# Performance work log

Hardware: AMD Instinct MI355X
Metric: run time of the kernel (lower is better)

The kernel has to match this reference:

```python
import jax, jax.numpy as jnp
import numpy as np

N_NODES = 50000
N_EDGES = 800000
IN_FEAT = 128
HID = 64
HEADS = 4
OUT = 40
NEG_SLOPE = 0.2


def _p(key, shape, scale=0.05):
    return jax.random.normal(key, shape, dtype=jnp.float32) * scale


def setup_inputs() -> dict:
    key = jax.random.key(0)
    ks = jax.random.split(key, 20)
    HW = HID * HEADS  # 256
    inp = {
        "x": jax.random.normal(ks[0], (N_NODES, IN_FEAT), dtype=jnp.float32),
        "edge_index": jax.random.randint(ks[1], (2, N_EDGES), 0, N_NODES, dtype=jnp.int64),
        # GATConv 1: in=128 -> heads=4, C=64
        "W1": _p(ks[2], (IN_FEAT, HW)), "as1": _p(ks[3], (HEADS, HID)), "ad1": _p(ks[4], (HEADS, HID)), "b1": jnp.zeros((HW,), jnp.float32),
        # GATConv 2: in=256
        "W2": _p(ks[5], (HW, HW)), "as2": _p(ks[6], (HEADS, HID)), "ad2": _p(ks[7], (HEADS, HID)), "b2": jnp.zeros((HW,), jnp.float32),
        # GATConv 3: in=256
        "W3": _p(ks[8], (HW, HW)), "as3": _p(ks[9], (HEADS, HID)), "ad3": _p(ks[10], (HEADS, HID)), "b3": jnp.zeros((HW,), jnp.float32),
        # MLP head: Linear(256,256) + Linear(256,40)
        "Wm1": _p(ks[11], (HW, HW)), "bm1": jnp.zeros((HW,), jnp.float32),
        "Wm2": _p(ks[12], (HW, OUT)), "bm2": jnp.zeros((OUT,), jnp.float32),
    }
    return inp


def gat_conv(x, src, dst, W, a_src, a_dst, bias, num_nodes):
    """PyG GATConv: concat=True, add_self_loops=True, leaky_relu(0.2)."""
    H, C = a_src.shape
    h = (x @ W).reshape(num_nodes, H, C)            # [N,H,C]
    # per-node attention logits (computed once, gathered per edge)
    src_logit = jnp.einsum('nhc,hc->nh', h, a_src)  # [N,H]
    dst_logit = jnp.einsum('nhc,hc->nh', h, a_dst)  # [N,H]
    # add self loops
    loop = jnp.arange(num_nodes, dtype=src.dtype)
    s = jnp.concatenate([src, loop])
    d = jnp.concatenate([dst, loop])
    alpha = jax.nn.leaky_relu(src_logit[s] + dst_logit[d], NEG_SLOPE)  # [E,H]
    # segment softmax over incoming edges of each destination node
    amax = jax.ops.segment_max(alpha, d, num_segments=num_nodes)
    e = jnp.exp(alpha - amax[d])
    denom = jax.ops.segment_sum(e, d, num_segments=num_nodes)
    coef = e / denom[d]                              # [E,H]
    msg = h[s] * coef[:, :, None]                    # [E,H,C] gather+weight
    out = jax.ops.segment_sum(msg, d, num_segments=num_nodes)  # [N,H,C]
    return out.reshape(num_nodes, H * C) + bias


def reference(x, edge_index, W1, as1, ad1, b1, W2, as2, ad2, b2, W3, as3, ad3, b3, Wm1, bm1, Wm2, bm2):
    src, dst = edge_index[0], edge_index[1]
    n = x.shape[0]
    h = jax.nn.relu(gat_conv(x, src, dst, W1, as1, ad1, b1, n))
    h = jax.nn.relu(gat_conv(h, src, dst, W2, as2, ad2, b2, n))
    h = jax.nn.relu(gat_conv(h, src, dst, W3, as3, ad3, b3, n))
    h = jax.nn.relu(h @ Wm1 + bm1)
    return h @ Wm2 + bm2
```

## Files before the change

### kernel.cpp

```cpp
#include <hip/hip_runtime.h>


constexpr int NN = 50000;
constexpr int NE = 800000;
constexpr int NN_PAD = 50176;
constexpr int CAP = 48;

typedef _Float16 f16x8 __attribute__((ext_vector_type(8)));
typedef _Float16 f16x4 __attribute__((ext_vector_type(4)));
typedef float    f32x4 __attribute__((ext_vector_type(4)));

__device__ __forceinline__ void cp16(void* lds, const void* g)
{
    __builtin_amdgcn_global_load_lds(
        (const __attribute__((address_space(1))) uint32_t*)g,
        (__attribute__((address_space(3))) uint32_t*)lds, 16, 0, 0);
}

constexpr int CVT_BLKS = 944;
__global__ __launch_bounds__(256)
void prep_kernel(const float* __restrict__ W1, const float* __restrict__ W2,
                 const float* __restrict__ W3, const float* __restrict__ Wm1,
                 const float* __restrict__ Wm2,
                 _Float16* B1h, _Float16* B1l, _Float16* B2h, _Float16* B2l,
                 _Float16* B3h, _Float16* B3l, _Float16* Bmh, _Float16* Bml,
                 _Float16* Whh, _Float16* Whl,
                 const int* __restrict__ src, const int* __restrict__ dst,
                 int* __restrict__ cursor, int* __restrict__ bucket)
{
    if (blockIdx.x >= CVT_BLKS) {
        int e = ((int)blockIdx.x - CVT_BLKS) * 256 + (int)threadIdx.x;
        if (e >= NE) return;
        int d = dst[e];
        int pos = atomicAdd(&cursor[d], 1);
        if (pos < CAP) bucket[d * CAP + pos] = src[e];
        return;
    }
    int idx = blockIdx.x * 256 + (int)threadIdx.x;
    const float* W; _Float16 *H, *Lo; int K, local;
    if (idx < 32768)       { W = W1;  H = B1h; Lo = B1l; K = 128; local = idx; }
    else if (idx < 98304)  { W = W2;  H = B2h; Lo = B2l; K = 256; local = idx - 32768; }
    else if (idx < 163840) { W = W3;  H = B3h; Lo = B3l; K = 256; local = idx - 98304; }
    else if (idx < 229376) { W = Wm1; H = Bmh; Lo = Bml; K = 256; local = idx - 163840; }
    else if (idx < 241664) {
        int l = idx - 229376; int n = l >> 8, k = l & 255;
        float v = (n < 40) ? Wm2[k * 40 + n] : 0.f;
        _Float16 h = (_Float16)v;
        Whh[l] = h; Whl[l] = (_Float16)(v - (float)h);
        return;
    } else return;
    int k = local >> 8, n = local & 255;
    float v = W[local];
    _Float16 h = (_Float16)v;
    H[n * K + k] = h;
    Lo[n * K + k] = (_Float16)(v - (float)h);
}

template<bool FUSE, bool PRESPLIT, bool EMIT_SPLIT>
__global__ __launch_bounds__(512, 4)
void gemm_mfma(const float* __restrict__ A,
               const _Float16* Ah, const _Float16* Al,
               const _Float16* __restrict__ Bhi, const _Float16* __restrict__ Blo,
               const float* __restrict__ bias,
               _Float16* __restrict__ h16, _Float16* __restrict__ h16lo,
               _Float16* Oh, _Float16* Ol,
               const float* __restrict__ a_src, const float* __restrict__ a_dst,
               float* __restrict__ sl, float* __restrict__ dl,
               int M, int K)
{
    __shared__ __align__(16) _Float16 sAhi[128][32], sAlo[128][32];
    __shared__ __align__(16) _Float16 sBhi[256][32], sBlo[256][32];

    const int tid  = (int)threadIdx.x;
    const int wave = tid >> 6;
    const int mw   = wave >> 2;
    const int nw   = wave & 3;
    const int lane = tid & 63;
    const int l15  = lane & 15;
    const int quad = lane >> 4;
    const int swz  = (l15 >> 1) & 3;
    const int bm   = blockIdx.x * 128;

    f32x4 acc[4][4];
    #pragma unroll
    for (int i = 0; i < 4; ++i)
        #pragma unroll
        for (int j = 0; j < 4; ++j)
            acc[i][j] = (f32x4){0.f, 0.f, 0.f, 0.f};

    for (int k0 = 0; k0 < K; k0 += 32) {
        {
            int pos = lane & 3;
            #pragma unroll
            for (int j = 0; j < 2; ++j) {
                int rowB = wave * 32 + j * 16 + (lane >> 2);
                int c = pos ^ ((rowB >> 1) & 3);
                cp16(&sBhi[wave * 32 + j * 16][0], Bhi + (size_t)rowB * K + k0 + c * 8);
                cp16(&sBlo[wave * 32 + j * 16][0], Blo + (size_t)rowB * K + k0 + c * 8);
            }
        }
        if (PRESPLIT) {
            int pos = lane & 3;
            int rowA = wave * 16 + (lane >> 2);
            int c = pos ^ ((rowA >> 1) & 3);
            cp16(&sAhi[wave * 16][0], Ah + (size_t)(bm + rowA) * K + k0 + c * 8);
            cp16(&sAlo[wave * 16][0], Al + (size_t)(bm + rowA) * K + k0 + c * 8);
        } else {
            int r = tid >> 2, c = tid & 3;
            int grow = bm + r;
            float4 v0 = make_float4(0.f, 0.f, 0.f, 0.f), v1 = v0;
            if (grow < M) {
                v0 = *(const float4*)(A + (size_t)grow * K + k0 + c * 8);
                v1 = *(const float4*)(A + (size_t)grow * K + k0 + c * 8 + 4);
            }
            float fv[8] = {v0.x, v0.y, v0.z, v0.w, v1.x, v1.y, v1.z, v1.w};
            f16x8 h8, l8;
            #pragma unroll
            for (int u = 0; u < 8; ++u) {
                _Float16 hh = (_Float16)fv[u];
                h8[u] = hh; l8[u] = (_Float16)(fv[u] - (float)hh);
            }
            int slot = (c ^ ((r >> 1) & 3)) * 8;
            *(f16x8*)&sAhi[r][slot] = h8;
            *(f16x8*)&sAlo[r][slot] = l8;
        }
        __syncthreads();

        f16x8 bh[4], bl[4];
        #pragma unroll
        for (int nt = 0; nt < 4; ++nt) {
            int n = nw * 64 + nt * 16 + l15;
            bh[nt] = *(const f16x8*)&sBhi[n][(quad ^ swz) * 8];
            bl[nt] = *(const f16x8*)&sBlo[n][(quad ^ swz) * 8];
        }
        #pragma unroll
        for (int mt = 0; mt < 4; ++mt) {
            int m = mw * 64 + mt * 16 + l15;
            f16x8 ah = *(const f16x8*)&sAhi[m][(quad ^ swz) * 8];
            f16x8 al = *(const f16x8*)&sAlo[m][(quad ^ swz) * 8];
            #pragma unroll
            for (int nt = 0; nt < 4; ++nt) {
                acc[mt][nt] = __builtin_amdgcn_mfma_f32_16x16x32_f16(ah, bh[nt], acc[mt][nt], 0, 0, 0);
                acc[mt][nt] = __builtin_amdgcn_mfma_f32_16x16x32_f16(al, bh[nt], acc[mt][nt], 0, 0, 0);
                acc[mt][nt] = __builtin_amdgcn_mfma_f32_16x16x32_f16(ah, bl[nt], acc[mt][nt], 0, 0, 0);
            }
        }
        __syncthreads();
    }

    float aS[4], aD[4];
    if (FUSE) {
        #pragma unroll
        for (int nt = 0; nt < 4; ++nt) {
            aS[nt] = a_src[nw * 64 + nt * 16 + l15];
            aD[nt] = a_dst[nw * 64 + nt * 16 + l15];
        }
    }

    #pragma unroll
    for (int mt = 0; mt < 4; ++mt) {
        #pragma unroll
        for (int r = 0; r < 4; ++r) {
            int row = bm + mw * 64 + mt * 16 + quad * 4 + r;
            bool ok = (row < M);
            if (ok) {
                #pragma unroll
                for (int nt = 0; nt < 4; ++nt) {
                    int col = nw * 64 + nt * 16 + l15;
                    float c = acc[mt][nt][r];
                    if (EMIT_SPLIT) {
                        float v = fmaxf(c + bias[col], 0.f);
                        _Float16 hh = (_Float16)v;
                        Oh[(size_t)row * 256 + col] = hh;
                        Ol[(size_t)row * 256 + col] = (_Float16)(v - (float)hh);
                    } else {
                        _Float16 hh = (_Float16)c;
                        h16[(size_t)row * 256 + col] = hh;
                        h16lo[(size_t)row * 256 + col] = (_Float16)(c - (float)hh);
                    }
                }
            }
            if (FUSE) {
                float vs = 0.f, vd = 0.f;
                #pragma unroll
                for (int nt = 0; nt < 4; ++nt) {
                    float c = acc[mt][nt][r];
                    vs = fmaf(c, aS[nt], vs);
                    vd = fmaf(c, aD[nt], vd);
                }
                #pragma unroll
                for (int off = 8; off >= 1; off >>= 1) {
                    vs += __shfl_xor(vs, off, 64);
                    vd += __shfl_xor(vd, off, 64);
                }
                if (l15 == 0 && ok) {
                    sl[row * 4 + nw] = vs;
                    dl[row * 4 + nw] = vd;
                }
            }
        }
    }
}

__global__ __launch_bounds__(256)
void gemm_head(const _Float16* __restrict__ Ah, const _Float16* __restrict__ Al,
               const _Float16* __restrict__ Bh, const _Float16* __restrict__ Bl,
               const float* __restrict__ bias, float* __restrict__ out, int M)
{
    __shared__ _Float16 sAhi[256][40], sAlo[256][40];
    __shared__ _Float16 sBhi[48][40],  sBlo[48][40];

    const int tid  = (int)threadIdx.x;
    const int wave = tid >> 6;
    const int lane = tid & 63;
    const int l15  = lane & 15;
    const int quad = lane >> 4;
    const int bm   = blockIdx.x * 256;

    f32x4 acc[4][3];
    #pragma unroll
    for (int i = 0; i < 4; ++i)
        #pragma unroll
        for (int j = 0; j < 3; ++j)
            acc[i][j] = (f32x4){0.f, 0.f, 0.f, 0.f};

    for (int k0 = 0; k0 < 256; k0 += 32) {
        #pragma unroll
        for (int i = 0; i < 4; ++i) {
            int idx = tid + i * 256;
            int row = idx >> 2, kq = (idx & 3) * 8;
            int grow = bm + row;
            uint4 vh = {0,0,0,0}, vl = {0,0,0,0};
            if (grow < M) {
                vh = *(const uint4*)(Ah + (size_t)grow * 256 + k0 + kq);
                vl = *(const uint4*)(Al + (size_t)grow * 256 + k0 + kq);
            }
            *(uint4*)&sAhi[row][kq] = vh;
            *(uint4*)&sAlo[row][kq] = vl;
        }
        if (tid < 192) {
            int n = tid >> 2, kq = (tid & 3) * 8;
            *(uint4*)&sBhi[n][kq] = *(const uint4*)(Bh + (size_t)n * 256 + k0 + kq);
            *(uint4*)&sBlo[n][kq] = *(const uint4*)(Bl + (size_t)n * 256 + k0 + kq);
        }
        __syncthreads();

        f16x8 bh[3], bl[3];
        #pragma unroll
        for (int nt = 0; nt < 3; ++nt) {
            int n = nt * 16 + l15;
            bh[nt] = *(const f16x8*)&sBhi[n][quad * 8];
            bl[nt] = *(const f16x8*)&sBlo[n][quad * 8];
        }
        #pragma unroll
        for (int mt = 0; mt < 4; ++mt) {
            int m = wave * 64 + mt * 16 + l15;
            f16x8 ah = *(const f16x8*)&sAhi[m][quad * 8];
            f16x8 al = *(const f16x8*)&sAlo[m][quad * 8];
            #pragma unroll
            for (int nt = 0; nt < 3; ++nt) {
                acc[mt][nt] = __builtin_amdgcn_mfma_f32_16x16x32_f16(ah, bh[nt], acc[mt][nt], 0, 0, 0);
                acc[mt][nt] = __builtin_amdgcn_mfma_f32_16x16x32_f16(al, bh[nt], acc[mt][nt], 0, 0, 0);
                acc[mt][nt] = __builtin_amdgcn_mfma_f32_16x16x32_f16(ah, bl[nt], acc[mt][nt], 0, 0, 0);
            }
        }
        __syncthreads();
    }

    #pragma unroll
    for (int mt = 0; mt < 4; ++mt) {
        #pragma unroll
        for (int r = 0; r < 4; ++r) {
            int row = bm + wave * 64 + mt * 16 + quad * 4 + r;
            if (row >= M) continue;
            #pragma unroll
            for (int nt = 0; nt < 3; ++nt) {
                int col = nt * 16 + l15;
                if (col < 40)
                    out[(size_t)row * 40 + col] = acc[mt][nt][r] + bias[col];
            }
        }
    }
}

__device__ __forceinline__ float leaky02(float a) {
    return (a >= 0.f) ? a : 0.2f * a;
}

__global__ __launch_bounds__(256)
void gat_aggregate(const int* __restrict__ cursor, const int* __restrict__ bucket,
                   const float* __restrict__ sl, const float* __restrict__ dl,
                   const _Float16* __restrict__ h16, const _Float16* __restrict__ h16lo,
                   const float* __restrict__ bias,
                   _Float16* __restrict__ Ph, _Float16* __restrict__ Pl)
{
    __shared__ __align__(16) float sE[4][CAP][4];
    __shared__ __align__(16) int   sIdx[4][CAP];

    const int wv = (int)threadIdx.x >> 6;
    const int n = blockIdx.x * 4 + wv;
    if (n >= NN) return;
    const int lane = (int)threadIdx.x & 63;
    const int head = lane >> 4;
    const int cnt = min(cursor[n], CAP);

    if (lane < cnt) {
        int s = bucket[(size_t)n * CAP + lane];
        sIdx[wv][lane] = s;
        float4 s4 = *(const float4*)(sl + s * 4);
        float4 d4 = *(const float4*)(dl + n * 4);
        float4 e4;
        e4.x = __expf(leaky02(s4.x + d4.x));
        e4.y = __expf(leaky02(s4.y + d4.y));
        e4.z = __expf(leaky02(s4.z + d4.z));
        e4.w = __expf(leaky02(s4.w + d4.w));
        *(float4*)&sE[wv][lane][0] = e4;
    }

    const float dlh = dl[n * 4 + head];
    float exs = __expf(leaky02(sl[n * 4 + head] + dlh));
    f16x4 shi = *(const f16x4*)(h16   + (size_t)n * 256 + lane * 4);
    f16x4 slo = *(const f16x4*)(h16lo + (size_t)n * 256 + lane * 4);
    float4 a0; float d0 = exs;
    a0.x = exs * ((float)shi[0] + (float)slo[0]);
    a0.y = exs * ((float)shi[1] + (float)slo[1]);
    a0.z = exs * ((float)shi[2] + (float)slo[2]);
    a0.w = exs * ((float)shi[3] + (float)slo[3]);
    float4 a1 = {0,0,0,0}, a2 = {0,0,0,0}, a3 = {0,0,0,0};
    float d1 = 0.f, d2 = 0.f, d3 = 0.f;

    const int vo = lane * 4;
    int i = 0;
    for (; i + 3 < cnt; i += 4) {
        int s0 = __builtin_amdgcn_readfirstlane(sIdx[wv][i]);
        int s1 = __builtin_amdgcn_readfirstlane(sIdx[wv][i + 1]);
        int s2 = __builtin_amdgcn_readfirstlane(sIdx[wv][i + 2]);
        int s3 = __builtin_amdgcn_readfirstlane(sIdx[wv][i + 3]);
        float e0 = sE[wv][i][head];
        float e1 = sE[wv][i + 1][head];
        float e2 = sE[wv][i + 2][head];
        float e3 = sE[wv][i + 3][head];
        f16x4 h0 = *(const f16x4*)(h16 + ((size_t)(uint32_t)s0 << 8) + vo);
        f16x4 h1 = *(const f16x4*)(h16 + ((size_t)(uint32_t)s1 << 8) + vo);
        f16x4 h2 = *(const f16x4*)(h16 + ((size_t)(uint32_t)s2 << 8) + vo);
        f16x4 h3 = *(const f16x4*)(h16 + ((size_t)(uint32_t)s3 << 8) + vo);
        a0.x = fmaf(e0, (float)h0[0], a0.x); a0.y = fmaf(e0, (float)h0[1], a0.y);
        a0.z = fmaf(e0, (float)h0[2], a0.z); a0.w = fmaf(e0, (float)h0[3], a0.w);
        d0 += e0;
        a1.x = fmaf(e1, (float)h1[0], a1.x); a1.y = fmaf(e1, (float)h1[1], a1.y);
        a1.z = fmaf(e1, (float)h1[2], a1.z); a1.w = fmaf(e1, (float)h1[3], a1.w);
        d1 += e1;
        a2.x = fmaf(e2, (float)h2[0], a2.x); a2.y = fmaf(e2, (float)h2[1], a2.y);
        a2.z = fmaf(e2, (float)h2[2], a2.z); a2.w = fmaf(e2, (float)h2[3], a2.w);
        d2 += e2;
        a3.x = fmaf(e3, (float)h3[0], a3.x); a3.y = fmaf(e3, (float)h3[1], a3.y);
        a3.z = fmaf(e3, (float)h3[2], a3.z); a3.w = fmaf(e3, (float)h3[3], a3.w);
        d3 += e3;
    }
    for (; i < cnt; ++i) {
        int s0 = __builtin_amdgcn_readfirstlane(sIdx[wv][i]);
        float e0 = sE[wv][i][head];
        f16x4 h0 = *(const f16x4*)(h16 + ((size_t)(uint32_t)s0 << 8) + vo);
        a0.x = fmaf(e0, (float)h0[0], a0.x); a0.y = fmaf(e0, (float)h0[1], a0.y);
        a0.z = fmaf(e0, (float)h0[2], a0.z); a0.w = fmaf(e0, (float)h0[3], a0.w);
        d0 += e0;
    }
    float4 acc;
    acc.x = (a0.x + a1.x) + (a2.x + a3.x);
    acc.y = (a0.y + a1.y) + (a2.y + a3.y);
    acc.z = (a0.z + a1.z) + (a2.z + a3.z);
    acc.w = (a0.w + a1.w) + (a2.w + a3.w);
    float denom = (d0 + d1) + (d2 + d3);

    float inv = 1.f / denom;
    float4 bv = *(const float4*)(bias + lane * 4);
    float rv[4];
    rv[0] = fmaxf(bv.x + acc.x * inv, 0.f);
    rv[1] = fmaxf(bv.y + acc.y * inv, 0.f);
    rv[2] = fmaxf(bv.z + acc.z * inv, 0.f);
    rv[3] = fmaxf(bv.w + acc.w * inv, 0.f);
    f16x4 h, l;
    #pragma unroll
    for (int u = 0; u < 4; ++u) {
        _Float16 hh = (_Float16)rv[u];
        h[u] = hh; l[u] = (_Float16)(rv[u] - (float)hh);
    }
    *(f16x4*)(Ph + (size_t)n * 256 + vo) = h;
    *(f16x4*)(Pl + (size_t)n * 256 + vo) = l;
}

extern "C" void kernel_launch(void* const* d_in, const int* in_sizes, int n_in,
                              void* d_out, int out_size, void* d_ws, size_t ws_size,
                              hipStream_t stream)
{
    const float* x   = (const float*)d_in[0];
    const int*   ei  = (const int*)d_in[1];
    const int* src = ei;
    const int* dst = ei + NE;
    const float* W1  = (const float*)d_in[2];
    const float* as1 = (const float*)d_in[3];
    const float* ad1 = (const float*)d_in[4];
    const float* b1  = (const float*)d_in[5];
    const float* W2  = (const float*)d_in[6];
    const float* as2 = (const float*)d_in[7];
    const float* ad2 = (const float*)d_in[8];
    const float* b2  = (const float*)d_in[9];
    const float* W3  = (const float*)d_in[10];
    const float* as3 = (const float*)d_in[11];
    const float* ad3 = (const float*)d_in[12];
    const float* b3  = (const float*)d_in[13];
    const float* Wm1 = (const float*)d_in[14];
    const float* bm1 = (const float*)d_in[15];
    const float* Wm2 = (const float*)d_in[16];
    const float* bm2 = (const float*)d_in[17];
    float* out = (float*)d_out;

    float* ws  = (float*)d_ws;
    float* sl  = ws;
    float* dl  = sl + NN * 4;
    int* cursor = (int*)(dl + NN * 4);
    int* bucket = cursor + NN;
    uintptr_t fb = (uintptr_t)(bucket + (size_t)NN * CAP);
    fb = (fb + 15) & ~(uintptr_t)15;
    _Float16* wb = (_Float16*)fb;
    _Float16* B1h = wb;                 _Float16* B1l = B1h + 256 * 128;
    _Float16* B2h = B1l + 256 * 128;    _Float16* B2l = B2h + 256 * 256;
    _Float16* B3h = B2l + 256 * 256;    _Float16* B3l = B3h + 256 * 256;
    _Float16* Bmh = B3l + 256 * 256;    _Float16* Bml = Bmh + 256 * 256;
    _Float16* Whh = Bml + 256 * 256;    _Float16* Whl = Whh + 48 * 256;
    _Float16* H16  = Whl + 48 * 256;
    _Float16* H16l = H16 + (size_t)NN * 256;
    _Float16* Ph  = H16l + (size_t)NN * 256;
    _Float16* Pl  = Ph   + (size_t)NN_PAD * 256;

    const dim3 block(256);
    const dim3 block512(512);
    const dim3 mfmaGrid((NN + 127) / 128);
    const dim3 headGrid((NN + 255) / 256);
    const int prepBlocks = CVT_BLKS + (NE + 255) / 256;
    const int aggBlocks = (NN + 3) / 4;

    (void)hipMemsetAsync(cursor, 0, (size_t)NN * sizeof(int), stream);
    prep_kernel<<<prepBlocks, block, 0, stream>>>(
        W1, W2, W3, Wm1, Wm2, B1h, B1l, B2h, B2l, B3h, B3l, Bmh, Bml, Whh, Whl,
        src, dst, cursor, bucket);

    gemm_mfma<true, false, false><<<mfmaGrid, block512, 0, stream>>>(
        x, nullptr, nullptr, B1h, B1l, nullptr, H16, H16l, nullptr, nullptr,
        as1, ad1, sl, dl, NN, 128);
    gat_aggregate<<<aggBlocks, block, 0, stream>>>(cursor, bucket, sl, dl, H16, H16l, b1, Ph, Pl);

    gemm_mfma<true, true, false><<<mfmaGrid, block512, 0, stream>>>(
        nullptr, Ph, Pl, B2h, B2l, nullptr, H16, H16l, nullptr, nullptr,
        as2, ad2, sl, dl, NN, 256);
    gat_aggregate<<<aggBlocks, block, 0, stream>>>(cursor, bucket, sl, dl, H16, H16l, b2, Ph, Pl);

    gemm_mfma<true, true, false><<<mfmaGrid, block512, 0, stream>>>(
        nullptr, Ph, Pl, B3h, B3l, nullptr, H16, H16l, nullptr, nullptr,
        as3, ad3, sl, dl, NN, 256);
    gat_aggregate<<<aggBlocks, block, 0, stream>>>(cursor, bucket, sl, dl, H16, H16l, b3, Ph, Pl);

    gemm_mfma<false, true, true><<<mfmaGrid, block512, 0, stream>>>(
        nullptr, Ph, Pl, Bmh, Bml, bm1, nullptr, nullptr, Ph, Pl,
        nullptr, nullptr, nullptr, nullptr, NN, 256);
    gemm_head<<<headGrid, block, 0, stream>>>(Ph, Pl, Whh, Whl, bm2, out, NN);
}
```

Baseline: 584.9 us.

## Double-buffer A tiles in MFMA GEMM to overlap loads with compute

Splits the A-operand shared-memory tiles into two buffers so the next K-slice of A is prefetched (via LDS DMA or register loads plus fp16 split) while MFMAs run on the current slice. B stays single-buffered and is reloaded between two barriers after compute. The aim is to hide global-load latency for A, at the cost of doubled A LDS usage and an extra barrier per iteration, with B loads still exposed.

```diff
diff --git a/kernel.cpp b/kernel.cpp
--- a/kernel.cpp
+++ b/kernel.cpp
@@ -68,7 +68,7 @@
                float* __restrict__ sl, float* __restrict__ dl,
                int M, int K)
 {
-    __shared__ __align__(16) _Float16 sAhi[128][32], sAlo[128][32];
+    __shared__ __align__(16) _Float16 sAhi[2][128][32], sAlo[2][128][32];
     __shared__ __align__(16) _Float16 sBhi[256][32], sBlo[256][32];
 
     const int tid  = (int)threadIdx.x;
@@ -88,43 +88,65 @@
         for (int j = 0; j < 4; ++j)
             acc[i][j] = (f32x4){0.f, 0.f, 0.f, 0.f};
 
-    for (int k0 = 0; k0 < K; k0 += 32) {
-        {
-            int pos = lane & 3;
-            #pragma unroll
-            for (int j = 0; j < 2; ++j) {
-                int rowB = wave * 32 + j * 16 + (lane >> 2);
-                int c = pos ^ ((rowB >> 1) & 3);
-                cp16(&sBhi[wave * 32 + j * 16][0], Bhi + (size_t)rowB * K + k0 + c * 8);
-                cp16(&sBlo[wave * 32 + j * 16][0], Blo + (size_t)rowB * K + k0 + c * 8);
-            }
-        }
-        if (PRESPLIT) {
-            int pos = lane & 3;
-            int rowA = wave * 16 + (lane >> 2);
-            int c = pos ^ ((rowA >> 1) & 3);
-            cp16(&sAhi[wave * 16][0], Ah + (size_t)(bm + rowA) * K + k0 + c * 8);
-            cp16(&sAlo[wave * 16][0], Al + (size_t)(bm + rowA) * K + k0 + c * 8);
-        } else {
-            int r = tid >> 2, c = tid & 3;
-            int grow = bm + r;
-            float4 v0 = make_float4(0.f, 0.f, 0.f, 0.f), v1 = v0;
-            if (grow < M) {
-                v0 = *(const float4*)(A + (size_t)grow * K + k0 + c * 8);
-                v1 = *(const float4*)(A + (size_t)grow * K + k0 + c * 8 + 4);
-            }
-            float fv[8] = {v0.x, v0.y, v0.z, v0.w, v1.x, v1.y, v1.z, v1.w};
-            f16x8 h8, l8;
-            #pragma unroll
-            for (int u = 0; u < 8; ++u) {
-                _Float16 hh = (_Float16)fv[u];
-                h8[u] = hh; l8[u] = (_Float16)(fv[u] - (float)hh);
-            }
-            int slot = (c ^ ((r >> 1) & 3)) * 8;
-            *(f16x8*)&sAhi[r][slot] = h8;
-            *(f16x8*)&sAlo[r][slot] = l8;
-        }
-        __syncthreads();
+    auto stageA_dma = [&](int b, int k0) {
+        int rowA = wave * 16 + (lane >> 2);
+        int c = (lane & 3) ^ ((rowA >> 1) & 3);
+        cp16(&sAhi[b][wave * 16][0], Ah + (size_t)(bm + rowA) * K + k0 + c * 8);
+        cp16(&sAlo[b][wave * 16][0], Al + (size_t)(bm + rowA) * K + k0 + c * 8);
+    };
+    auto stageB = [&](int k0) {
+        int pos = lane & 3;
+        #pragma unroll
+        for (int j = 0; j < 2; ++j) {
+            int rowB = wave * 32 + j * 16 + (lane >> 2);
+            int c = pos ^ ((rowB >> 1) & 3);
+            cp16(&sBhi[wave * 32 + j * 16][0], Bhi + (size_t)rowB * K + k0 + c * 8);
+            cp16(&sBlo[wave * 32 + j * 16][0], Blo + (size_t)rowB * K + k0 + c * 8);
+        }
+    };
+    const int ar = tid >> 2, ac = tid & 3;
+    auto writeA_cvt = [&](int b, float4 v0, float4 v1) {
+        float fv[8] = {v0.x, v0.y, v0.z, v0.w, v1.x, v1.y, v1.z, v1.w};
+        f16x8 h8, l8;
+        #pragma unroll
+        for (int u = 0; u < 8; ++u) {
+            _Float16 hh = (_Float16)fv[u];
+            h8[u] = hh; l8[u] = (_Float16)(fv[u] - (float)hh);
+        }
+        int slot = (ac ^ ((ar >> 1) & 3)) * 8;
+        *(f16x8*)&sAhi[b][ar][slot] = h8;
+        *(f16x8*)&sAlo[b][ar][slot] = l8;
+    };
+    auto loadA32 = [&](int k0, float4& v0, float4& v1) {
+        int grow = bm + ar;
+        v0 = make_float4(0.f, 0.f, 0.f, 0.f); v1 = v0;
+        if (grow < M) {
+            v0 = *(const float4*)(A + (size_t)grow * K + k0 + ac * 8);
+            v1 = *(const float4*)(A + (size_t)grow * K + k0 + ac * 8 + 4);
+        }
+    };
+
+    if (PRESPLIT) {
+        stageA_dma(0, 0);
+    } else {
+        float4 v0, v1;
+        loadA32(0, v0, v1);
+        writeA_cvt(0, v0, v1);
+    }
+    stageB(0);
+    __syncthreads();
+
+    const int NT = K >> 5;
+    for (int t = 0; t < NT; ++t) {
+        const int cb = t & 1, nb = cb ^ 1;
+        const bool pf = (t + 1 < NT);
+        const int kn = (t + 1) << 5;
+
+        float4 pv0, pv1;
+        if (pf) {
+            if (PRESPLIT) stageA_dma(nb, kn);
+            else          loadA32(kn, pv0, pv1);
+        }
 
         f16x8 bh[4], bl[4];
         #pragma unroll
@@ -136,8 +158,8 @@
         #pragma unroll
         for (int mt = 0; mt < 4; ++mt) {
             int m = mw * 64 + mt * 16 + l15;
-            f16x8 ah = *(const f16x8*)&sAhi[m][(quad ^ swz) * 8];
-            f16x8 al = *(const f16x8*)&sAlo[m][(quad ^ swz) * 8];
+            f16x8 ah = *(const f16x8*)&sAhi[cb][m][(quad ^ swz) * 8];
+            f16x8 al = *(const f16x8*)&sAlo[cb][m][(quad ^ swz) * 8];
             #pragma unroll
             for (int nt = 0; nt < 4; ++nt) {
                 acc[mt][nt] = __builtin_amdgcn_mfma_f32_16x16x32_f16(ah, bh[nt], acc[mt][nt], 0, 0, 0);
@@ -145,7 +167,14 @@
                 acc[mt][nt] = __builtin_amdgcn_mfma_f32_16x16x32_f16(ah, bl[nt], acc[mt][nt], 0, 0, 0);
             }
         }
-        __syncthreads();
+
+        if (pf && !PRESPLIT) writeA_cvt(nb, pv0, pv1);
+
+        if (pf) {
+            __syncthreads();
+            stageB(kn);
+            __syncthreads();
+        }
     }
 
     float aS[4], aD[4];
```

After: 568.3 us. -2.8%, faster.
